# Optimization experiments

Hardware: AMD Instinct MI355X
Metric: run time of the kernel (lower is better)

## Reference

```python
import jax, jax.numpy as jnp
import numpy as np

B, S, D, H = 2, 2048, 1024, 16
HD = D // H  # head_dim = 64

def setup_inputs() -> dict:
    key = jax.random.key(0)
    ks = jax.random.split(key, 6)
    sc = 0.02
    return {
        "x": jax.random.normal(ks[0], (B, S, D), dtype=jnp.float32),
        "Wq": jax.random.normal(ks[1], (D, D), dtype=jnp.float32) * sc,
        "Wk": jax.random.normal(ks[2], (D, D), dtype=jnp.float32) * sc,
        "Wv": jax.random.normal(ks[3], (D, D), dtype=jnp.float32) * sc,
        "Wo": jax.random.normal(ks[4], (D, D), dtype=jnp.float32) * sc,
        "bo": jnp.zeros((D,), dtype=jnp.float32),
    }

def reference(x, Wq, Wk, Wv, Wo, bo):
    b, s, d = x.shape
    # QKV projections (no bias, qkv_bias=False)
    q = (x @ Wq).reshape(b, s, H, HD).transpose(0, 2, 1, 3)  # [b,h,s,hd]
    k = (x @ Wk).reshape(b, s, H, HD).transpose(0, 2, 1, 3)
    v = (x @ Wv).reshape(b, s, H, HD).transpose(0, 2, 1, 3)
    scores = jnp.einsum("bhqd,bhkd->bhqk", q, k)  # [b,h,s,s]
    causal = jnp.triu(jnp.ones((s, s), dtype=bool), k=1)
    scores = jnp.where(causal, -jnp.inf, scores)
    # NOTE: source divides by keys.shape[-1]**0 / 5 == 1/5 -> scores / 5 (faithful)
    attn = jax.nn.softmax(scores / 5.0, axis=-1)
    ctx = jnp.einsum("bhqk,bhkd->bhqd", attn, v)  # [b,h,s,hd]
    ctx = ctx.transpose(0, 2, 1, 3).reshape(b, s, d)
    return ctx @ Wo + bo
```

## Files before the change

### kernel.cpp

```cpp
#include <hip/hip_runtime.h>
#include <math.h>

#define BB 2
#define SS 2048
#define DD 1024
#define HH 16
#define HD 64
#define MM (BB*SS)

typedef float  f32x4 __attribute__((ext_vector_type(4)));
typedef short  s16x8 __attribute__((ext_vector_type(8)));
typedef unsigned short u16;
typedef u16    u16x4 __attribute__((ext_vector_type(4)));
typedef unsigned int u32;
typedef u32    u32x2 __attribute__((ext_vector_type(2)));
typedef u32    u32x4 __attribute__((ext_vector_type(4)));

static __device__ __forceinline__ u16 f2bf(float f) {
    u32 u = __float_as_uint(f);
    u = (u + 0x7FFFu + ((u >> 16) & 1u)) >> 16;
    return (u16)u;
}

static __device__ __forceinline__ u32 cvtpk_bf16(float lo, float hi) {
    u32 r;
    asm("v_cvt_pk_bf16_f32 %0, %1, %2" : "=v"(r) : "v"(lo), "v"(hi));
    return r;
}

static __device__ __forceinline__ void gload16(const u16* g, void* l) {
    __builtin_amdgcn_global_load_lds((const __attribute__((address_space(1))) u32*)g,
                                     (__attribute__((address_space(3))) u32*)l, 16, 0, 0);
}

__global__ __launch_bounds__(256) void conv_x(const float* __restrict__ in,
                                              u16* __restrict__ outb) {
    int i = blockIdx.x * 256 + threadIdx.x;
    const f32x4* p = (const f32x4*)in;
    f32x4 a = p[i*2], b = p[i*2 + 1];
    u16x4 lo, hi;
    lo[0]=f2bf(a.x); lo[1]=f2bf(a.y); lo[2]=f2bf(a.z); lo[3]=f2bf(a.w);
    hi[0]=f2bf(b.x); hi[1]=f2bf(b.y); hi[2]=f2bf(b.z); hi[3]=f2bf(b.w);
    *(u16x4*)(outb + (size_t)i*8)     = lo;
    *(u16x4*)(outb + (size_t)i*8 + 4) = hi;
}

__global__ __launch_bounds__(256) void conv_wt(const float* __restrict__ W0,
                                               const float* __restrict__ W1,
                                               const float* __restrict__ W2,
                                               const float* __restrict__ W3,
                                               u16* __restrict__ WT) {
    const int z = blockIdx.z;
    const float* W = (z==0) ? W0 : (z==1) ? W1 : (z==2) ? W2 : W3;
    u16* dst = WT + (size_t)z * 1024 * 1024;
    __shared__ u16 tr[64][72];
    const int t = threadIdx.x;
    const int r0 = blockIdx.y * 64, c0 = blockIdx.x * 64;
    #pragma unroll
    for (int u = 0; u < 4; ++u) {
        int idx = u*256 + t;
        int r = idx >> 4, c4 = (idx & 15) * 4;
        f32x4 v = *(const f32x4*)(W + (size_t)(r0 + r)*1024 + c0 + c4);
        tr[c4+0][r] = f2bf(v.x);
        tr[c4+1][r] = f2bf(v.y);
        tr[c4+2][r] = f2bf(v.z);
        tr[c4+3][r] = f2bf(v.w);
    }
    __syncthreads();
    {
        int c = t >> 2, rq = (t & 3) * 16;
        u32x4 v0 = *(const u32x4*)&tr[c][rq];
        u32x4 v1 = *(const u32x4*)&tr[c][rq + 8];
        u16* op = dst + (size_t)(c0 + c)*1024 + r0 + rq;
        *(u32x4*)op       = v0;
        *(u32x4*)(op + 8) = v1;
    }
}

template<int EPI, int NJ>
__global__ __launch_bounds__(256) void mfma_gemm(const u16* __restrict__ A,
                                                 const u16* __restrict__ WT,
                                                 const float* __restrict__ bias,
                                                 u16* __restrict__ Qb,
                                                 u16* __restrict__ Kb,
                                                 u16* __restrict__ Vtb,
                                                 float* __restrict__ outF) {
    constexpr int BN = NJ * 32;
    __shared__ u32x4 smemv[2048];
    char* smem = (char*)smemv;
    char* Bsm  = smem + 16384;
    const int t   = threadIdx.x;
    const int w   = t >> 6;
    const int l   = t & 63;
    const int c15 = l & 15;
    const int g16 = ((l >> 4) & 3) << 4;
    const int mw  = w >> 1, nw = w & 1;
    const int brow = blockIdx.y * 128;
    const int bcol = blockIdx.x * BN;

    f32x4 acc[4][NJ] = {};

    const u16* Asrc = A  + (size_t)brow * DD;
    const u16* Bsrc = WT + (size_t)bcol * DD;

    for (int k0 = 0; k0 < DD; k0 += 64) {
        #pragma unroll
        for (int u = 0; u < 4; ++u) {
            int idx = u*256 + t;
            int row = idx >> 3;
            int cb  = (idx & 7) << 4;
            int off = (cb ^ ((row & 7) << 4)) >> 1;
            gload16(Asrc + (size_t)row*DD + k0 + off, smem + ((idx - l) << 4));
        }
        #pragma unroll
        for (int u = 0; u < NJ; ++u) {
            int idx = u*256 + t;
            int row = idx >> 3;
            int cb  = (idx & 7) << 4;
            int off = (cb ^ ((row & 7) << 4)) >> 1;
            gload16(Bsrc + (size_t)row*DD + k0 + off, Bsm + ((idx - l) << 4));
        }
        __syncthreads();

        s16x8 af[4][2], bf[NJ][2];
        #pragma unroll
        for (int mi = 0; mi < 4; ++mi) {
            int row = mw*64 + mi*16 + c15;
            int sw  = (row & 7) << 4;
            af[mi][0] = *(const s16x8*)(smem + row*128 + ((g16)      ^ sw));
            af[mi][1] = *(const s16x8*)(smem + row*128 + ((64 + g16) ^ sw));
        }
        #pragma unroll
        for (int nj = 0; nj < NJ; ++nj) {
            int row = nw*(NJ*16) + nj*16 + c15;
            int sw  = (row & 7) << 4;
            bf[nj][0] = *(const s16x8*)(Bsm + row*128 + ((g16)      ^ sw));
            bf[nj][1] = *(const s16x8*)(Bsm + row*128 + ((64 + g16) ^ sw));
        }
        #pragma unroll
        for (int c = 0; c < 2; ++c)
            #pragma unroll
            for (int mi = 0; mi < 4; ++mi)
                #pragma unroll
                for (int nj = 0; nj < NJ; ++nj)
                    acc[mi][nj] = __builtin_amdgcn_mfma_f32_16x16x32_bf16(
                        af[mi][c], bf[nj][c], acc[mi][nj], 0, 0, 0);
        __syncthreads();
    }

    if constexpr (EPI == 1) {
        #pragma unroll
        for (int mi = 0; mi < 4; ++mi)
            #pragma unroll
            for (int r = 0; r < 4; ++r) {
                int mg = brow + mw*64 + mi*16 + ((l >> 4) & 3)*4 + r;
                #pragma unroll
                for (int nj = 0; nj < NJ; ++nj) {
                    int nc = bcol + nw*(NJ*16) + nj*16 + c15;
                    outF[(size_t)mg*DD + nc] = acc[mi][nj][r] + bias[nc];
                }
            }
    } else {
        const int wq   = blockIdx.x >> 3;
        const int ncw0 = (blockIdx.x & 7)*128 + nw*64;
        if (wq < 2) {
            u16* dst  = wq ? Kb : Qb;
            float scl = wq ? 1.0f : 0.28853900817779268f;
            #pragma unroll
            for (int mi = 0; mi < 4; ++mi)
                #pragma unroll
                for (int r = 0; r < 4; ++r) {
                    int mg = brow + mw*64 + mi*16 + ((l >> 4) & 3)*4 + r;
                    int b_ = mg >> 11, s_ = mg & (SS-1);
                    #pragma unroll
                    for (int nj = 0; nj < NJ; ++nj) {
                        int nc = ncw0 + nj*16 + c15;
                        int h_ = nc >> 6, d_ = nc & 63;
                        dst[(((size_t)b_*HH + h_)*SS + s_)*HD + d_] =
                            f2bf(acc[mi][nj][r] * scl);
                    }
                }
        } else {
            char* tw = smem + w*8192;
            #pragma unroll
            for (int nj = 0; nj < NJ; ++nj)
                #pragma unroll
                for (int mi = 0; mi < 4; ++mi)
                    #pragma unroll
                    for (int r = 0; r < 4; ++r) {
                        int n = nj*16 + c15;
                        int m = mi*16 + ((l >> 4) & 3)*4 + r;
                        *(u16*)(tw + n*128 + ((m*2) ^ ((n & 7) << 4))) =
                            f2bf(acc[mi][nj][r]);
                    }
            __syncthreads();
            #pragma unroll
            for (int it = 0; it < 8; ++it) {
                int n  = it*8 + (l >> 3);
                int mb = l & 7;
                u32x4 v = *(const u32x4*)(tw + n*128 + ((mb*16) ^ ((n & 7) << 4)));
                int nc = ncw0 + n;
                int h_ = nc >> 6, d_ = nc & 63;
                int mg0 = brow + mw*64;
                int b_ = mg0 >> 11;
                int sb = (mg0 & (SS-1)) + mb*8;
                *(u32x4*)(Vtb + (((size_t)b_*HH + h_)*HD + d_)*SS + sb) = v;
            }
        }
    }
}

__global__ __launch_bounds__(512) void attn_mfma(const u16* __restrict__ Q,
                                                 const u16* __restrict__ K,
                                                 const u16* __restrict__ Vt,
                                                 u16* __restrict__ ctx) {
    __shared__ u32x4 smemv[6144];
    char* smem = (char*)smemv;
    const int pr = blockIdx.x;
    const int h  = blockIdx.y;
    const int b  = blockIdx.z;
    const int t  = threadIdx.x;
    const int w  = t >> 6;
    const int l  = t & 63;
    const int g  = l >> 4;
    const int q15 = l & 15;
    char* Psm = smem + 65536 + w*4096;

    const size_t bh = ((size_t)b*HH + h) * SS;
    const u16* Kg = K  + bh * HD;
    const u16* Vg = Vt + ((size_t)(b*HH + h)) * HD * SS;

    #pragma unroll 1
    for (int half = 0; half < 2; ++half) {
        const int qb = half ? (15 - pr) : pr;
        const u16* Qw = Q + (bh + (size_t)qb*128 + w*16 + q15) * HD;
        s16x8 qf0 = *(const s16x8*)(Qw + g*8);
        s16x8 qf1 = *(const s16x8*)(Qw + 32 + g*8);

        f32x4 acc[4] = {};
        float m = -1e30f, lsum = 0.f;
        const int qg = qb*128 + w*16 + q15;

        u32x4 kreg[2], vreg[2];
        #pragma unroll
        for (int u = 0; u < 2; ++u) {
            int idx = u*512 + t;
            kreg[u] = *(const u32x4*)(Kg + (size_t)(idx >> 3)*HD + (idx & 7)*8);
            vreg[u] = *(const u32x4*)(Vg + (size_t)(idx >> 4)*SS + (idx & 15)*8);
        }
        if (half) __syncthreads();
        #pragma unroll
        for (int u = 0; u < 2; ++u) {
            int idx = u*512 + t;
            int kr = idx >> 3, kc = (idx & 7) << 4;
            *(u32x4*)(smem + kr*128 + (kc ^ ((kr & 7) << 4))) = kreg[u];
            int vr = idx >> 4, vc = (idx & 15) << 4;
            *(u32x4*)(smem + 32768 + vr*256 + (vc ^ ((vr & 7) << 4))) = vreg[u];
        }

        int cur = 0;
        for (int kt = 0; kt <= qb; ++kt) {
            const bool pf = (kt < qb);
            if (pf) {
                #pragma unroll
                for (int u = 0; u < 2; ++u) {
                    int idx = u*512 + t;
                    kreg[u] = *(const u32x4*)(Kg + (size_t)((kt+1)*128 + (idx >> 3))*HD + (idx & 7)*8);
                    vreg[u] = *(const u32x4*)(Vg + (size_t)(idx >> 4)*SS + (kt+1)*128 + (idx & 15)*8);
                }
            }
            __syncthreads();
            char* Kc = smem + (cur << 14);
            char* Vc = smem + 32768 + (cur << 14);

            f32x4 st[8];
            __builtin_amdgcn_s_setprio(1);
            #pragma unroll
            for (int kb = 0; kb < 8; ++kb) {
                f32x4 z = {0.f, 0.f, 0.f, 0.f};
                int row = kb*16 + q15;
                int sw  = (row & 7) << 4;
                s16x8 a0 = *(const s16x8*)(Kc + row*128 + ((g*16)      ^ sw));
                s16x8 a1 = *(const s16x8*)(Kc + row*128 + ((64 + g*16) ^ sw));
                z = __builtin_amdgcn_mfma_f32_16x16x32_bf16(a0, qf0, z, 0, 0, 0);
                z = __builtin_amdgcn_mfma_f32_16x16x32_bf16(a1, qf1, z, 0, 0, 0);
                st[kb] = z;
            }
            __builtin_amdgcn_s_setprio(0);

            if (kt == qb) {
                #pragma unroll
                for (int kb = 0; kb < 8; ++kb)
                    #pragma unroll
                    for (int r = 0; r < 4; ++r) {
                        int key = kt*128 + kb*16 + g*4 + r;
                        if (key > qg) st[kb][r] = -1e30f;
                    }
            }

            float tmax = -1e30f;
            #pragma unroll
            for (int kb = 0; kb < 8; ++kb)
                #pragma unroll
                for (int r = 0; r < 4; ++r) tmax = fmaxf(tmax, st[kb][r]);
            tmax = fmaxf(tmax, __shfl_xor(tmax, 16));
            tmax = fmaxf(tmax, __shfl_xor(tmax, 32));
            float mnew = fmaxf(m, tmax);
            float scl  = __builtin_amdgcn_exp2f(m - mnew);
            float ps = 0.f;
            #pragma unroll
            for (int kb = 0; kb < 8; ++kb)
                #pragma unroll
                for (int r = 0; r < 4; ++r) {
                    float p = __builtin_amdgcn_exp2f(st[kb][r] - mnew);
                    st[kb][r] = p;
                    ps += p;
                }
            ps += __shfl_xor(ps, 16);
            ps += __shfl_xor(ps, 32);
            lsum = lsum * scl + ps;
            m = mnew;

            #pragma unroll
            for (int r = 0; r < 4; ++r) {
                float sr = __shfl(scl, g*4 + r);
                #pragma unroll
                for (int n = 0; n < 4; ++n) acc[n][r] *= sr;
            }

            {
                int swp = (q15 & 7) << 4;
                #pragma unroll
                for (int kb = 0; kb < 8; ++kb) {
                    u32x2 pk2;
                    pk2[0] = cvtpk_bf16(st[kb][0], st[kb][1]);
                    pk2[1] = cvtpk_bf16(st[kb][2], st[kb][3]);
                    *(u32x2*)(Psm + q15*256 + ((kb*32 + g*8) ^ swp)) = pk2;
                }
                s16x8 pa[4];
                #pragma unroll
                for (int c = 0; c < 4; ++c)
                    pa[c] = *(const s16x8*)(Psm + q15*256 + ((c*64 + g*16) ^ swp));
                __builtin_amdgcn_s_setprio(1);
                #pragma unroll
                for (int n = 0; n < 4; ++n) {
                    int row = n*16 + q15;
                    int sw  = (row & 7) << 4;
                    #pragma unroll
                    for (int c = 0; c < 4; ++c) {
                        s16x8 vv = *(const s16x8*)(Vc + row*256 + ((c*64 + g*16) ^ sw));
                        acc[n] = __builtin_amdgcn_mfma_f32_16x16x32_bf16(pa[c], vv, acc[n], 0, 0, 0);
                    }
                }
                __builtin_amdgcn_s_setprio(0);
            }

            if (pf) {
                char* Kn = smem + ((cur ^ 1) << 14);
                char* Vn = smem + 32768 + ((cur ^ 1) << 14);
                #pragma unroll
                for (int u = 0; u < 2; ++u) {
                    int idx = u*512 + t;
                    int kr = idx >> 3, kc = (idx & 7) << 4;
                    *(u32x4*)(Kn + kr*128 + (kc ^ ((kr & 7) << 4))) = kreg[u];
                    int vr = idx >> 4, vc = (idx & 15) << 4;
                    *(u32x4*)(Vn + vr*256 + (vc ^ ((vr & 7) << 4))) = vreg[u];
                }
            }
            cur ^= 1;
        }

        #pragma unroll
        for (int r = 0; r < 4; ++r) {
            float inv = 1.f / __shfl(lsum, g*4 + r);
            int qrow = qb*128 + w*16 + g*4 + r;
            u16* crow = ctx + ((size_t)b*SS + qrow)*DD + h*HD;
            #pragma unroll
            for (int n = 0; n < 4; ++n)
                crow[n*16 + q15] = f2bf(acc[n][r] * inv);
        }
    }
}

extern "C" void kernel_launch(void* const* d_in, const int* in_sizes, int n_in,
                              void* d_out, int out_size, void* d_ws, size_t ws_size,
                              hipStream_t stream) {
    const float* x  = (const float*)d_in[0];
    const float* Wq = (const float*)d_in[1];
    const float* Wk = (const float*)d_in[2];
    const float* Wv = (const float*)d_in[3];
    const float* Wo = (const float*)d_in[4];
    const float* bo = (const float*)d_in[5];
    float* out = (float*)d_out;

    const size_t NELT = (size_t)MM * DD;
    const size_t NW   = (size_t)1024 * 1024;
    u16* wsb  = (u16*)d_ws;
    u16* xb   = wsb;
    u16* WT   = wsb + NELT;
    u16* Qb   = wsb + NELT + 4*NW;
    u16* Kb   = Qb + NELT;
    u16* Vtb  = Kb + NELT;
    u16* Ctxb = Vtb + NELT;
    u16* WTqkv = WT;
    u16* WTo   = WT + 3*NW;

    hipLaunchKernelGGL(conv_x, dim3(2048), dim3(256), 0, stream, x, xb);
    hipLaunchKernelGGL(conv_wt, dim3(16,16,4), dim3(256), 0, stream, Wq, Wk, Wv, Wo, WT);

    hipLaunchKernelGGL((mfma_gemm<0,4>), dim3(24,32), dim3(256), 0, stream,
                       xb, WTqkv, nullptr, Qb, Kb, Vtb, nullptr);

    hipLaunchKernelGGL(attn_mfma, dim3(8,16,2), dim3(512), 0, stream, Qb, Kb, Vtb, Ctxb);

    hipLaunchKernelGGL((mfma_gemm<1,2>), dim3(16,32), dim3(256), 0, stream,
                       Ctxb, WTo, bo, nullptr, nullptr, nullptr, out);
}
```

Baseline: 112.2 us.

## Double-buffer GEMM shared memory to overlap global loads with MFMA

Splits the GEMM k-loop into stage and compute lambdas over two LDS buffers, so the next tile's global-to-LDS loads are issued before computing on the current tile. This hides global load latency behind the MFMA work and drops one barrier per k-step. The cost is double the LDS footprint, which may reduce occupancy.

```diff
diff --git a/kernel.cpp b/kernel.cpp
--- a/kernel.cpp
+++ b/kernel.cpp
@@ -85,10 +85,15 @@
                                                  u16* __restrict__ Kb,
                                                  u16* __restrict__ Vtb,
                                                  float* __restrict__ outF) {
-    constexpr int BN = NJ * 32;
-    __shared__ u32x4 smemv[2048];
+    constexpr int BN  = NJ * 32;
+    constexpr int ASZ = 16384;
+    constexpr int BSZ = NJ * 4096;
+    __shared__ u32x4 smemv[(2*(ASZ + BSZ))/16];
     char* smem = (char*)smemv;
-    char* Bsm  = smem + 16384;
+    char* A0 = smem;
+    char* B0 = smem + ASZ;
+    char* A1 = smem + ASZ + BSZ;
+    char* B1 = smem + 2*ASZ + BSZ;
     const int t   = threadIdx.x;
     const int w   = t >> 6;
     const int l   = t & 63;
@@ -103,14 +108,14 @@
     const u16* Asrc = A  + (size_t)brow * DD;
     const u16* Bsrc = WT + (size_t)bcol * DD;
 
-    for (int k0 = 0; k0 < DD; k0 += 64) {
+    auto stage = [&](int k0, char* Ab, char* Bb) {
         #pragma unroll
         for (int u = 0; u < 4; ++u) {
             int idx = u*256 + t;
             int row = idx >> 3;
             int cb  = (idx & 7) << 4;
             int off = (cb ^ ((row & 7) << 4)) >> 1;
-            gload16(Asrc + (size_t)row*DD + k0 + off, smem + ((idx - l) << 4));
+            gload16(Asrc + (size_t)row*DD + k0 + off, Ab + ((idx - l) << 4));
         }
         #pragma unroll
         for (int u = 0; u < NJ; ++u) {
@@ -118,24 +123,25 @@
             int row = idx >> 3;
             int cb  = (idx & 7) << 4;
             int off = (cb ^ ((row & 7) << 4)) >> 1;
-            gload16(Bsrc + (size_t)row*DD + k0 + off, Bsm + ((idx - l) << 4));
-        }
-        __syncthreads();
-
+            gload16(Bsrc + (size_t)row*DD + k0 + off, Bb + ((idx - l) << 4));
+        }
+    };
+
+    auto compute = [&](char* Ab, char* Bb) {
         s16x8 af[4][2], bf[NJ][2];
         #pragma unroll
         for (int mi = 0; mi < 4; ++mi) {
             int row = mw*64 + mi*16 + c15;
             int sw  = (row & 7) << 4;
-            af[mi][0] = *(const s16x8*)(smem + row*128 + ((g16)      ^ sw));
-            af[mi][1] = *(const s16x8*)(smem + row*128 + ((64 + g16) ^ sw));
+            af[mi][0] = *(const s16x8*)(Ab + row*128 + ((g16)      ^ sw));
+            af[mi][1] = *(const s16x8*)(Ab + row*128 + ((64 + g16) ^ sw));
         }
         #pragma unroll
         for (int nj = 0; nj < NJ; ++nj) {
             int row = nw*(NJ*16) + nj*16 + c15;
             int sw  = (row & 7) << 4;
-            bf[nj][0] = *(const s16x8*)(Bsm + row*128 + ((g16)      ^ sw));
-            bf[nj][1] = *(const s16x8*)(Bsm + row*128 + ((64 + g16) ^ sw));
+            bf[nj][0] = *(const s16x8*)(Bb + row*128 + ((g16)      ^ sw));
+            bf[nj][1] = *(const s16x8*)(Bb + row*128 + ((64 + g16) ^ sw));
         }
         #pragma unroll
         for (int c = 0; c < 2; ++c)
@@ -145,6 +151,16 @@
                 for (int nj = 0; nj < NJ; ++nj)
                     acc[mi][nj] = __builtin_amdgcn_mfma_f32_16x16x32_bf16(
                         af[mi][c], bf[nj][c], acc[mi][nj], 0, 0, 0);
+    };
+
+    stage(0, A0, B0);
+    __syncthreads();
+    for (int k0 = 0; k0 < DD; k0 += 128) {
+        stage(k0 + 64, A1, B1);
+        compute(A0, B0);
+        __syncthreads();
+        if (k0 + 128 < DD) stage(k0 + 128, A0, B0);
+        compute(A1, B1);
         __syncthreads();
     }
 
```

Result: faster. 101.6 us (-9.5%).
